# Kernel optimization log

Hardware: AMD Instinct MI355X
Metric: run time of the kernel (lower is better)

## Reference

```python
import jax, jax.numpy as jnp
import numpy as np

B, D = 65536, 154

def setup_inputs() -> dict:
    key = jax.random.key(0)
    k1, k2, k3, k4, k5, k6 = jax.random.split(key, 6)
    recon_l = jax.random.normal(k1, (B, D), dtype=jnp.float32)
    recon_r = jax.random.normal(k2, (B, D), dtype=jnp.float32)
    KLD_l = jax.random.normal(k3, (B, D), dtype=jnp.float32)
    KLD_r = jax.random.normal(k4, (B, D), dtype=jnp.float32)
    lr = jax.random.randint(k5, (B,), 0, 3, dtype=jnp.int64)
    # f_pose in {-1, 0}: -1 marks invalid samples
    f_pose = jax.random.randint(k6, (B,), 0, 2, dtype=jnp.int64) - 1
    return {"recon_l": recon_l, "recon_r": recon_r, "KLD_l": KLD_l,
            "KLD_r": KLD_r, "lr": lr, "f_pose": f_pose}

def reference(recon_l, recon_r, KLD_l, KLD_r, lr, f_pose):
    valid = (f_pose != -1)
    use_l = (valid & ((lr == 0) | (lr == 2))).astype(recon_l.dtype)  # [B]
    use_r = (valid & ((lr == 1) | (lr == 2))).astype(recon_r.dtype)  # [B]
    # per-sample sums over 154-dim pose params, then masked batch reduction
    recon_loss_all = jnp.dot(use_l, recon_l.sum(axis=1)) + jnp.dot(use_r, recon_r.sum(axis=1))
    KLD_loss_all = jnp.dot(use_l, KLD_l.sum(axis=1)) + jnp.dot(use_r, KLD_r.sum(axis=1))
    count = (use_l.sum() + use_r.sum()).astype(jnp.int32)
    return (recon_loss_all / 154.0, KLD_loss_all, count)
```

## Files before the change

### kernel.cpp

```cpp
#include <hip/hip_runtime.h>


#define BB 65536
#define DD 154
#define N4 (BB * DD / 4)
#define MAIN_BLOCKS 1232
#define MAIN_THREADS 256
#define TSTRIDE (MAIN_BLOCKS * MAIN_THREADS)
#define ITERS 8

__global__ void zero_out_kernel(float* __restrict__ out) {
    if (threadIdx.x < 3) out[threadIdx.x] = 0.0f;
}

__device__ __forceinline__ float2 wpair(int l, int f) {
    const bool valid = (f != -1);
    float2 w;
    w.x = (valid && ((l == 0) || (l == 2))) ? 1.0f : 0.0f;
    w.y = (valid && ((l == 1) || (l == 2))) ? 1.0f : 0.0f;
    return w;
}

__global__ __launch_bounds__(MAIN_THREADS) void pose_loss_kernel(
    const float* __restrict__ recon_l, const float* __restrict__ recon_r,
    const float* __restrict__ kld_l,   const float* __restrict__ kld_r,
    const int* __restrict__ lr,        const int* __restrict__ fp,
    float* __restrict__ out)
{
    const float4* __restrict__ rl4 = (const float4*)recon_l;
    const float4* __restrict__ rr4 = (const float4*)recon_r;
    const float4* __restrict__ kl4 = (const float4*)kld_l;
    const float4* __restrict__ kr4 = (const float4*)kld_r;

    const int t = blockIdx.x * MAIN_THREADS + threadIdx.x;

    float acc_recon = 0.0f, acc_kld = 0.0f, acc_cnt = 0.0f;

#pragma unroll
    for (int it = 0; it < ITERS; ++it) {
        const int i  = t + it * TSTRIDE;
        const int h  = 2 * i;
        const int r0 = h / 77;
        const int r1 = (h + 1) / 77;

        const float2 w0 = wpair(lr[r0], fp[r0]);
        const float2 w1 = wpair(lr[r1], fp[r1]);

        const float4 a = rl4[i];
        const float4 b = rr4[i];
        const float4 c = kl4[i];
        const float4 d = kr4[i];

        acc_recon += w0.x * (a.x + a.y) + w1.x * (a.z + a.w)
                   + w0.y * (b.x + b.y) + w1.y * (b.z + b.w);
        acc_kld   += w0.x * (c.x + c.y) + w1.x * (c.z + c.w)
                   + w0.y * (d.x + d.y) + w1.y * (d.z + d.w);
    }

    if (t < BB) {
        const float2 w = wpair(lr[t], fp[t]);
        acc_cnt = w.x + w.y;
    }

#pragma unroll
    for (int off = 32; off > 0; off >>= 1) {
        acc_recon += __shfl_down(acc_recon, off, 64);
        acc_kld   += __shfl_down(acc_kld,   off, 64);
        acc_cnt   += __shfl_down(acc_cnt,   off, 64);
    }

    __shared__ float s_recon[4], s_kld[4], s_cnt[4];
    const int wave = threadIdx.x >> 6;
    const int lane = threadIdx.x & 63;
    if (lane == 0) {
        s_recon[wave] = acc_recon;
        s_kld[wave]   = acc_kld;
        s_cnt[wave]   = acc_cnt;
    }
    __syncthreads();

    if (threadIdx.x == 0) {
        const float r = s_recon[0] + s_recon[1] + s_recon[2] + s_recon[3];
        const float k = s_kld[0]   + s_kld[1]   + s_kld[2]   + s_kld[3];
        const float c = s_cnt[0]   + s_cnt[1]   + s_cnt[2]   + s_cnt[3];
        atomicAdd(&out[0], r * (1.0f / 154.0f));
        atomicAdd(&out[1], k);
        atomicAdd(&out[2], c);
    }
}

extern "C" void kernel_launch(void* const* d_in, const int* in_sizes, int n_in,
                              void* d_out, int out_size, void* d_ws, size_t ws_size,
                              hipStream_t stream) {
    const float* recon_l = (const float*)d_in[0];
    const float* recon_r = (const float*)d_in[1];
    const float* kld_l   = (const float*)d_in[2];
    const float* kld_r   = (const float*)d_in[3];
    const int*   lr      = (const int*)d_in[4];
    const int*   fp      = (const int*)d_in[5];
    float* out = (float*)d_out;

    zero_out_kernel<<<1, 64, 0, stream>>>(out);
    pose_loss_kernel<<<MAIN_BLOCKS, MAIN_THREADS, 0, stream>>>(
        recon_l, recon_r, kld_l, kld_r, lr, fp, out);
}
```

Baseline: 189.4 us.

## Use one-float4-per-thread blocks with workspace partials and a final reduce kernel

The grid-stride loop of 8 iterations per thread is replaced by 9856 blocks where each thread loads one float4 from each input. Per-block partial sums go to a workspace array and a single 1024-thread kernel reduces them, replacing the zero kernel and global atomics when a workspace is available. This aims to raise memory-level parallelism and remove atomic contention, at the cost of more blocks, an extra kernel launch and less latency hiding per thread.

```diff
diff --git a/kernel.cpp b/kernel.cpp
--- a/kernel.cpp
+++ b/kernel.cpp
@@ -4,10 +4,8 @@
 #define BB 65536
 #define DD 154
 #define N4 (BB * DD / 4)
-#define MAIN_BLOCKS 1232
-#define MAIN_THREADS 256
-#define TSTRIDE (MAIN_BLOCKS * MAIN_THREADS)
-#define ITERS 8
+#define BLOCKS 9856
+#define THREADS 256
 
 __global__ void zero_out_kernel(float* __restrict__ out) {
     if (threadIdx.x < 3) out[threadIdx.x] = 0.0f;
@@ -21,44 +19,37 @@
     return w;
 }
 
-__global__ __launch_bounds__(MAIN_THREADS) void pose_loss_kernel(
+__global__ __launch_bounds__(THREADS) void pose_partial_kernel(
     const float* __restrict__ recon_l, const float* __restrict__ recon_r,
     const float* __restrict__ kld_l,   const float* __restrict__ kld_r,
     const int* __restrict__ lr,        const int* __restrict__ fp,
-    float* __restrict__ out)
+    float* __restrict__ ws,            float* __restrict__ out)
 {
     const float4* __restrict__ rl4 = (const float4*)recon_l;
     const float4* __restrict__ rr4 = (const float4*)recon_r;
     const float4* __restrict__ kl4 = (const float4*)kld_l;
     const float4* __restrict__ kr4 = (const float4*)kld_r;
 
-    const int t = blockIdx.x * MAIN_THREADS + threadIdx.x;
+    const int i = blockIdx.x * THREADS + threadIdx.x;
+    const int h = 2 * i;
+    const int r0 = h / 77;
+    const int r1 = (h + 1) / 77;
 
-    float acc_recon = 0.0f, acc_kld = 0.0f, acc_cnt = 0.0f;
+    const float4 a = rl4[i];
+    const float4 b = rr4[i];
+    const float4 c = kl4[i];
+    const float4 d = kr4[i];
 
-#pragma unroll
-    for (int it = 0; it < ITERS; ++it) {
-        const int i  = t + it * TSTRIDE;
-        const int h  = 2 * i;
-        const int r0 = h / 77;
-        const int r1 = (h + 1) / 77;
+    const float2 w0 = wpair(lr[r0], fp[r0]);
+    const float2 w1 = wpair(lr[r1], fp[r1]);
 
-        const float2 w0 = wpair(lr[r0], fp[r0]);
-        const float2 w1 = wpair(lr[r1], fp[r1]);
-
-        const float4 a = rl4[i];
-        const float4 b = rr4[i];
-        const float4 c = kl4[i];
-        const float4 d = kr4[i];
-
-        acc_recon += w0.x * (a.x + a.y) + w1.x * (a.z + a.w)
-                   + w0.y * (b.x + b.y) + w1.y * (b.z + b.w);
-        acc_kld   += w0.x * (c.x + c.y) + w1.x * (c.z + c.w)
-                   + w0.y * (d.x + d.y) + w1.y * (d.z + d.w);
-    }
-
-    if (t < BB) {
-        const float2 w = wpair(lr[t], fp[t]);
+    float acc_recon = w0.x * (a.x + a.y) + w1.x * (a.z + a.w)
+                    + w0.y * (b.x + b.y) + w1.y * (b.z + b.w);
+    float acc_kld   = w0.x * (c.x + c.y) + w1.x * (c.z + c.w)
+                    + w0.y * (d.x + d.y) + w1.y * (d.z + d.w);
+    float acc_cnt = 0.0f;
+    if (i < BB) {
+        const float2 w = wpair(lr[i], fp[i]);
         acc_cnt = w.x + w.y;
     }
 
@@ -82,10 +73,46 @@
     if (threadIdx.x == 0) {
         const float r = s_recon[0] + s_recon[1] + s_recon[2] + s_recon[3];
         const float k = s_kld[0]   + s_kld[1]   + s_kld[2]   + s_kld[3];
-        const float c = s_cnt[0]   + s_cnt[1]   + s_cnt[2]   + s_cnt[3];
-        atomicAdd(&out[0], r * (1.0f / 154.0f));
-        atomicAdd(&out[1], k);
-        atomicAdd(&out[2], c);
+        const float n = s_cnt[0]   + s_cnt[1]   + s_cnt[2]   + s_cnt[3];
+        if (ws != nullptr) {
+            ws[blockIdx.x]              = r;
+            ws[BLOCKS + blockIdx.x]     = k;
+            ws[2 * BLOCKS + blockIdx.x] = n;
+        } else {
+            atomicAdd(&out[0], r * (1.0f / 154.0f));
+            atomicAdd(&out[1], k);
+            atomicAdd(&out[2], n);
+        }
+    }
+}
+
+__global__ __launch_bounds__(1024) void final_reduce_kernel(
+    const float* __restrict__ ws, float* __restrict__ out)
+{
+    float r = 0.0f, k = 0.0f, n = 0.0f;
+    for (int i = threadIdx.x; i < BLOCKS; i += 1024) {
+        r += ws[i];
+        k += ws[BLOCKS + i];
+        n += ws[2 * BLOCKS + i];
+    }
+#pragma unroll
+    for (int off = 32; off > 0; off >>= 1) {
+        r += __shfl_down(r, off, 64);
+        k += __shfl_down(k, off, 64);
+        n += __shfl_down(n, off, 64);
+    }
+    __shared__ float s_r[16], s_k[16], s_n[16];
+    const int wave = threadIdx.x >> 6;
+    const int lane = threadIdx.x & 63;
+    if (lane == 0) { s_r[wave] = r; s_k[wave] = k; s_n[wave] = n; }
+    __syncthreads();
+    if (threadIdx.x == 0) {
+        float rr = 0.0f, kk = 0.0f, nn = 0.0f;
+#pragma unroll
+        for (int w = 0; w < 16; ++w) { rr += s_r[w]; kk += s_k[w]; nn += s_n[w]; }
+        out[0] = rr * (1.0f / 154.0f);
+        out[1] = kk;
+        out[2] = nn;
     }
 }
 
@@ -100,7 +127,16 @@
     const int*   fp      = (const int*)d_in[5];
     float* out = (float*)d_out;
 
-    zero_out_kernel<<<1, 64, 0, stream>>>(out);
-    pose_loss_kernel<<<MAIN_BLOCKS, MAIN_THREADS, 0, stream>>>(
-        recon_l, recon_r, kld_l, kld_r, lr, fp, out);
+    const bool use_ws = (d_ws != nullptr) &&
+                        (ws_size >= (size_t)(3 * BLOCKS) * sizeof(float));
+    float* ws = use_ws ? (float*)d_ws : nullptr;
+
+    if (!use_ws) {
+        zero_out_kernel<<<1, 64, 0, stream>>>(out);
+    }
+    pose_partial_kernel<<<BLOCKS, THREADS, 0, stream>>>(
+        recon_l, recon_r, kld_l, kld_r, lr, fp, ws, out);
+    if (use_ws) {
+        final_reduce_kernel<<<1, 1024, 0, stream>>>(ws, out);
+    }
 }
```

After: 178.5 us. 5.7% less time.
